# Kernel tuning notes

Hardware: AMD Instinct MI355X
Metric: run time of the kernel (lower is better)

Reference implementation:

```python
import jax, jax.numpy as jnp
import numpy as np
import math

N_HEADS = 12
EPS = 1e-5

def _layernorm(x, w, b):
    # torch .var() is unbiased (ddof=1)
    mean = jnp.mean(x, axis=-1, keepdims=True)
    var = jnp.var(x, axis=-1, keepdims=True, ddof=1)
    return (x - mean) / jnp.sqrt(var + EPS) * w + b

def _gelu_tanh(x):
    c = math.sqrt(2.0 / math.pi)
    return 0.5 * x * (1.0 + jnp.tanh(c * (x + 0.044715 * x * x * x)))

def setup_inputs() -> dict:
    key = jax.random.key(0)
    ks = jax.random.split(key, 6)
    B, T, C = 4, 2048, 768
    s = 0.02
    return {
        "x": jax.random.normal(ks[0], (B, T, C), jnp.float32),
        "ln1_w": jnp.ones((C,), jnp.float32),
        "ln1_b": jnp.zeros((C,), jnp.float32),
        "c_attn_w": jax.random.normal(ks[1], (C, 3 * C), jnp.float32) * s,
        "c_attn_b": jnp.zeros((3 * C,), jnp.float32),
        "c_proj_w": jax.random.normal(ks[2], (C, C), jnp.float32) * s,
        "c_proj_b": jnp.zeros((C,), jnp.float32),
        "ln2_w": jnp.ones((C,), jnp.float32),
        "ln2_b": jnp.zeros((C,), jnp.float32),
        "fc_w": jax.random.normal(ks[3], (C, 4 * C), jnp.float32) * s,
        "fc_b": jnp.zeros((4 * C,), jnp.float32),
        "mproj_w": jax.random.normal(ks[4], (4 * C, C), jnp.float32) * s,
        "mproj_b": jnp.zeros((C,), jnp.float32),
    }

def _attention(x, c_attn_w, c_attn_b, c_proj_w, c_proj_b):
    B, T, C = x.shape
    H = N_HEADS
    D = C // H
    qkv = x @ c_attn_w + c_attn_b  # [B,T,3C]
    q, k, v = jnp.split(qkv, 3, axis=-1)
    q = q.reshape(B, T, H, D).transpose(0, 2, 1, 3)  # [B,H,T,D]
    k = k.reshape(B, T, H, D).transpose(0, 2, 1, 3)
    v = v.reshape(B, T, H, D).transpose(0, 2, 1, 3)
    scores = jnp.einsum("bhqd,bhkd->bhqk", q, k) * (D ** -0.5)  # [B,H,T,T]
    causal = jnp.tril(jnp.ones((T, T), bool))
    scores = jnp.where(causal[None, None], scores, jnp.float32(-jnp.inf))
    attn = jax.nn.softmax(scores, axis=-1)
    out = jnp.einsum("bhqk,bhkd->bhqd", attn, v)  # [B,H,T,D]
    out = out.transpose(0, 2, 1, 3).reshape(B, T, C)
    return out @ c_proj_w + c_proj_b

def reference(x, ln1_w, ln1_b, c_attn_w, c_attn_b, c_proj_w, c_proj_b,
              ln2_w, ln2_b, fc_w, fc_b, mproj_w, mproj_b):
    x = x + _attention(_layernorm(x, ln1_w, ln1_b), c_attn_w, c_attn_b, c_proj_w, c_proj_b)
    h = _gelu_tanh(_layernorm(x, ln2_w, ln2_b) @ fc_w + fc_b)
    return x + h @ mproj_w + mproj_b
```

## Files before the change

kernel.cpp:

```cpp
#include <hip/hip_runtime.h>
#include <hip/hip_bf16.h>
#include <cstdint>

#define BF __hip_bfloat16

typedef __bf16 v8bf __attribute__((ext_vector_type(8)));
typedef float  v4f  __attribute__((ext_vector_type(4)));

__device__ __forceinline__ float tof(BF v) { return __bfloat162float(v); }
__device__ __forceinline__ BF    tob(float v) { return __float2bfloat16(v); }
__device__ __forceinline__ float ldf(float v) { return v; }
__device__ __forceinline__ float ldf(BF v) { return tof(v); }
__device__ __forceinline__ void stv(float* p, float v) { *p = v; }
__device__ __forceinline__ void stv(BF* p, float v) { *p = tob(v); }

__device__ __forceinline__ v4f mfma16(v8bf a, v8bf b, v4f c) {
  return __builtin_amdgcn_mfma_f32_16x16x32_bf16(a, b, c, 0, 0, 0);
}

__device__ __forceinline__ void async16(const BF* g, BF* l) {
  __builtin_amdgcn_global_load_lds((const __attribute__((address_space(1))) void*)g,
                                   (__attribute__((address_space(3))) void*)l, 16, 0, 0);
}

__global__ __launch_bounds__(256) void transpose_k(const float* __restrict__ in,
                                                   BF* __restrict__ out, int R, int C) {
  __shared__ BF t[64][65];
  int tid = threadIdx.x;
  int c0 = blockIdx.x * 64, r0 = blockIdx.y * 64;
#pragma unroll
  for (int i = 0; i < 16; ++i) {
    int idx = i * 256 + tid;
    int rr = idx >> 6, cc = idx & 63;
    t[rr][cc] = tob(in[(size_t)(r0 + rr) * C + c0 + cc]);
  }
  __syncthreads();
#pragma unroll
  for (int i = 0; i < 16; ++i) {
    int idx = i * 256 + tid;
    int rr = idx >> 6, cc = idx & 63;
    out[(size_t)(c0 + rr) * R + r0 + cc] = t[cc][rr];
  }
}

__global__ __launch_bounds__(256) void vtrans_k(const BF* __restrict__ qkv,
                                                BF* __restrict__ vT) {
  __shared__ BF t[64][65];
  int tid = threadIdx.x;
  int t0 = blockIdx.x * 64;
  int bh = blockIdx.y;
  int b = bh / 12, h = bh % 12;
  const BF* src = qkv + (size_t)(b * 2048 + t0) * 2304 + 1536 + h * 64;
#pragma unroll
  for (int i = 0; i < 16; ++i) {
    int idx = i * 256 + tid;
    int rr = idx >> 6, cc = idx & 63;
    t[rr][cc] = src[(size_t)rr * 2304 + cc];
  }
  __syncthreads();
  BF* dst = vT + (size_t)bh * 64 * 2048 + t0;
#pragma unroll
  for (int i = 0; i < 16; ++i) {
    int idx = i * 256 + tid;
    int rr = idx >> 6, cc = idx & 63;
    dst[(size_t)rr * 2048 + cc] = t[cc][rr];
  }
}

template <typename TX>
__global__ __launch_bounds__(256) void ln_k(const TX* __restrict__ x,
                                            const float* __restrict__ w,
                                            const float* __restrict__ bia,
                                            BF* __restrict__ y) {
  int row = blockIdx.x, tid = threadIdx.x;
  const TX* xr = x + (size_t)row * 768;
  float v0 = ldf(xr[tid]), v1 = ldf(xr[tid + 256]), v2 = ldf(xr[tid + 512]);
  float s1 = v0 + v1 + v2;
  float s2 = v0 * v0 + v1 * v1 + v2 * v2;
#pragma unroll
  for (int m = 32; m; m >>= 1) { s1 += __shfl_xor(s1, m); s2 += __shfl_xor(s2, m); }
  __shared__ float rs[4][2];
  int wv = tid >> 6;
  if ((tid & 63) == 0) { rs[wv][0] = s1; rs[wv][1] = s2; }
  __syncthreads();
  s1 = rs[0][0] + rs[1][0] + rs[2][0] + rs[3][0];
  s2 = rs[0][1] + rs[1][1] + rs[2][1] + rs[3][1];
  float mean = s1 * (1.0f / 768.0f);
  float var = fmaxf((s2 - s1 * mean) * (1.0f / 767.0f), 0.0f);
  float rstd = rsqrtf(var + 1e-5f);
  BF* yr = y + (size_t)row * 768;
  yr[tid]       = tob((v0 - mean) * rstd * w[tid]       + bia[tid]);
  yr[tid + 256] = tob((v1 - mean) * rstd * w[tid + 256] + bia[tid + 256]);
  yr[tid + 512] = tob((v2 - mean) * rstd * w[tid + 512] + bia[tid + 512]);
}

__device__ __forceinline__ float gelu_f(float x) {
  float u = 0.7978845608028654f * (x + 0.044715f * x * x * x);
  float e = exp2f(2.8853900817779268f * u);
  return 0.5f * x * (1.0f + (1.0f - 2.0f / (e + 1.0f)));
}

template <int BN, int ACT, bool RESID, typename TR, typename TO>
__global__ __launch_bounds__(256) void gemm_bt_k(
    const BF* __restrict__ A, const BF* __restrict__ Bt, const float* __restrict__ bias,
    const TR* __restrict__ resid, TO* __restrict__ out, int M, int N, int K) {
  constexpr int NW = BN / 32;
  __shared__ __align__(16) BF As[128 * 32];
  __shared__ __align__(16) BF Bs[BN * 32];
  const int tid = threadIdx.x;
  const int w = tid >> 6, lane = tid & 63;
  const int quad = lane >> 4, l16 = lane & 15;
  const int m0 = blockIdx.y * 128, n0 = blockIdx.x * BN;
  const int wm = (w >> 1) * 64, wn = (w & 1) * (BN / 2);
  const int srow = lane >> 2, scol = (lane & 3) * 8;

  v4f acc[4][NW];
#pragma unroll
  for (int i = 0; i < 4; ++i)
#pragma unroll
    for (int j = 0; j < NW; ++j) acc[i][j] = (v4f){0.f, 0.f, 0.f, 0.f};

  for (int k0 = 0; k0 < K; k0 += 32) {
    __syncthreads();
#pragma unroll
    for (int i = 0; i < 2; ++i) {
      int c = w * 2 + i;
      async16(A + (size_t)(m0 + c * 16 + srow) * K + k0 + scol, &As[c * 512]);
    }
    if (BN == 128) {
#pragma unroll
      for (int i = 0; i < 2; ++i) {
        int c = w * 2 + i;
        async16(Bt + (size_t)(n0 + c * 16 + srow) * K + k0 + scol, &Bs[c * 512]);
      }
    } else {
      async16(Bt + (size_t)(n0 + w * 16 + srow) * K + k0 + scol, &Bs[w * 512]);
    }
    __syncthreads();
    v8bf af[4], bfv[NW];
#pragma unroll
    for (int mi = 0; mi < 4; ++mi)
      af[mi] = *(const v8bf*)&As[(wm + mi * 16 + l16) * 32 + quad * 8];
#pragma unroll
    for (int nj = 0; nj < NW; ++nj)
      bfv[nj] = *(const v8bf*)&Bs[(wn + nj * 16 + l16) * 32 + quad * 8];
#pragma unroll
    for (int mi = 0; mi < 4; ++mi)
#pragma unroll
      for (int nj = 0; nj < NW; ++nj)
        acc[mi][nj] = mfma16(af[mi], bfv[nj], acc[mi][nj]);
  }

#pragma unroll
  for (int nj = 0; nj < NW; ++nj) {
    int col = n0 + wn + nj * 16 + l16;
    float bv = bias[col];
#pragma unroll
    for (int mi = 0; mi < 4; ++mi) {
      v4f c = acc[mi][nj];
#pragma unroll
      for (int r = 0; r < 4; ++r) {
        int row = m0 + wm + mi * 16 + quad * 4 + r;
        float v = c[r] + bv;
        if (RESID) v += ldf(resid[(size_t)row * N + col]);
        if (ACT == 1) v = gelu_f(v);
        stv(&out[(size_t)row * N + col], v);
      }
    }
  }
}

__global__ __launch_bounds__(256) void attn_k(const BF* __restrict__ qkv,
                                              const BF* __restrict__ vT,
                                              BF* __restrict__ out) {
  __shared__ __align__(16) BF Ks[64 * 64];
  __shared__ __align__(16) BF Vs[64 * 64];
  __shared__ __align__(16) BF Ps[4][16 * 64];
  const int tid = threadIdx.x;
  const int w = tid >> 6, lane = tid & 63;
  const int quad = lane >> 4, l16 = lane & 15;
  const int bid = blockIdx.x;
  const int qi = 31 - (bid / 48);
  const int bh = bid % 48;
  const int b = bh / 12, h = bh % 12;
  const int q0 = qi * 64;
  const int qf = q0 + w * 16;
  BF* Pw = &Ps[w][0];
  const float L2E = 1.4426950408889634f;

  auto sz = [](int r, int c) { return (r << 6) + (c ^ ((r & 7) << 3)); };

  const BF* qp = qkv + (size_t)(b * 2048 + qf + l16) * 2304 + h * 64;
  v8bf q0v = *(const v8bf*)(qp + quad * 8);
  v8bf q1v = *(const v8bf*)(qp + 32 + quad * 8);
#pragma unroll
  for (int i = 0; i < 8; ++i) {
    q0v[i] = (__bf16)(tof((BF)q0v[i]) * 0.125f);
    q1v[i] = (__bf16)(tof((BF)q1v[i]) * 0.125f);
  }
  v8bf ones;
#pragma unroll
  for (int i = 0; i < 8; ++i) ones[i] = (__bf16)1.0f;

  v4f O[4], S;
#pragma unroll
  for (int j = 0; j < 4; ++j) O[j] = (v4f){0.f, 0.f, 0.f, 0.f};
  S = (v4f){0.f, 0.f, 0.f, 0.f};

  const BF* kg = qkv + (size_t)b * 2048 * 2304 + 768 + h * 64;
  const BF* vg = vT + (size_t)bh * 64 * 2048;
  const int r0 = tid >> 3, c0 = (tid & 7) * 8;
  const int r1 = r0 + 32;
  const int nIter = qi + 1;

  v8bf nk0 = *(const v8bf*)(kg + (size_t)r0 * 2304 + c0);
  v8bf nk1 = *(const v8bf*)(kg + (size_t)r1 * 2304 + c0);
  v8bf nv0 = *(const v8bf*)(vg + (size_t)r0 * 2048 + c0);
  v8bf nv1 = *(const v8bf*)(vg + (size_t)r1 * 2048 + c0);

  for (int t = 0; t < nIter; ++t) {
    const int kt0 = t * 64;
    __syncthreads();
    *(v8bf*)&Ks[sz(r0, c0)] = nk0;
    *(v8bf*)&Ks[sz(r1, c0)] = nk1;
    *(v8bf*)&Vs[sz(r0, c0)] = nv0;
    *(v8bf*)&Vs[sz(r1, c0)] = nv1;
    __syncthreads();
    if (t + 1 < nIter) {
      const int kn = kt0 + 64;
      nk0 = *(const v8bf*)(kg + (size_t)(kn + r0) * 2304 + c0);
      nk1 = *(const v8bf*)(kg + (size_t)(kn + r1) * 2304 + c0);
      nv0 = *(const v8bf*)(vg + (size_t)r0 * 2048 + kn + c0);
      nv1 = *(const v8bf*)(vg + (size_t)r1 * 2048 + kn + c0);
    }
    v4f s[4];
    __builtin_amdgcn_s_setprio(1);
#pragma unroll
    for (int nt = 0; nt < 4; ++nt) {
      v8bf kf0 = *(const v8bf*)&Ks[sz(nt * 16 + l16, quad * 8)];
      v8bf kf1 = *(const v8bf*)&Ks[sz(nt * 16 + l16, 32 + quad * 8)];
      s[nt] = mfma16(q1v, kf1, mfma16(q0v, kf0, (v4f){0.f, 0.f, 0.f, 0.f}));
    }
    __builtin_amdgcn_s_setprio(0);
    if (t < qi) {
#pragma unroll
      for (int nt = 0; nt < 4; ++nt)
#pragma unroll
        for (int r = 0; r < 4; ++r)
          Pw[sz(quad * 4 + r, nt * 16 + l16)] = tob(exp2f(s[nt][r] * L2E));
    } else {
#pragma unroll
      for (int nt = 0; nt < 4; ++nt) {
        int key = kt0 + nt * 16 + l16;
#pragma unroll
        for (int r = 0; r < 4; ++r) {
          int qrow = qf + quad * 4 + r;
          float p = (key <= qrow) ? exp2f(s[nt][r] * L2E) : 0.f;
          Pw[sz(quad * 4 + r, nt * 16 + l16)] = tob(p);
        }
      }
    }
    asm volatile("s_waitcnt lgkmcnt(0)" ::: "memory");
    v8bf p0 = *(const v8bf*)&Pw[sz(l16, quad * 8)];
    v8bf p1 = *(const v8bf*)&Pw[sz(l16, 32 + quad * 8)];
    __builtin_amdgcn_s_setprio(1);
#pragma unroll
    for (int j = 0; j < 4; ++j) {
      v8bf vf0 = *(const v8bf*)&Vs[sz(j * 16 + l16, quad * 8)];
      v8bf vf1 = *(const v8bf*)&Vs[sz(j * 16 + l16, 32 + quad * 8)];
      O[j] = mfma16(p1, vf1, mfma16(p0, vf0, O[j]));
    }
    S = mfma16(p1, ones, mfma16(p0, ones, S));
    __builtin_amdgcn_s_setprio(0);
  }

#pragma unroll
  for (int r = 0; r < 4; ++r) {
    float inv = 1.0f / S[r];
    int row = b * 2048 + qf + quad * 4 + r;
    BF* op = out + (size_t)row * 768 + h * 64 + l16;
#pragma unroll
    for (int j = 0; j < 4; ++j) op[j * 16] = tob(O[j][r] * inv);
  }
}

extern "C" void kernel_launch(void* const* d_in, const int* in_sizes, int n_in,
                              void* d_out, int out_size, void* d_ws, size_t ws_size,
                              hipStream_t stream) {
  const float* x        = (const float*)d_in[0];
  const float* ln1_w    = (const float*)d_in[1];
  const float* ln1_b    = (const float*)d_in[2];
  const float* c_attn_w = (const float*)d_in[3];
  const float* c_attn_b = (const float*)d_in[4];
  const float* c_proj_w = (const float*)d_in[5];
  const float* c_proj_b = (const float*)d_in[6];
  const float* ln2_w    = (const float*)d_in[7];
  const float* ln2_b    = (const float*)d_in[8];
  const float* fc_w     = (const float*)d_in[9];
  const float* fc_b     = (const float*)d_in[10];
  const float* mproj_w  = (const float*)d_in[11];
  const float* mproj_b  = (const float*)d_in[12];
  float* out = (float*)d_out;
  char* wsb = (char*)d_ws;
  dim3 blk(256);

  BF* vT = (BF*)((char*)d_out + 12582912);

  const size_t NEED_BIG = 89653248;
  if (ws_size >= NEED_BIG) {
    BF* qkv      = (BF*)(wsb);
    BF* hbuf     = (BF*)(wsb);
    BF* x2       = (BF*)(wsb + 50331648);
    BF* wT_attn  = (BF*)(wsb + 62914560);
    BF* wT_proj  = (BF*)(wsb + 66453504);
    BF* wT_fc    = (BF*)(wsb + 67633152);
    BF* wT_mproj = (BF*)(wsb + 72351744);
    BF* lnbuf    = (BF*)(wsb + 77070336);
    BF* attnout  = (BF*)d_out;

    transpose_k<<<dim3(36, 12), blk, 0, stream>>>(c_attn_w, wT_attn, 768, 2304);
    transpose_k<<<dim3(12, 12), blk, 0, stream>>>(c_proj_w, wT_proj, 768, 768);
    transpose_k<<<dim3(48, 12), blk, 0, stream>>>(fc_w, wT_fc, 768, 3072);
    transpose_k<<<dim3(12, 48), blk, 0, stream>>>(mproj_w, wT_mproj, 3072, 768);

    ln_k<float><<<8192, blk, 0, stream>>>(x, ln1_w, ln1_b, lnbuf);
    gemm_bt_k<128, 0, false, float, BF><<<dim3(18, 64), blk, 0, stream>>>(
        lnbuf, wT_attn, c_attn_b, (const float*)nullptr, qkv, 8192, 2304, 768);
    vtrans_k<<<dim3(32, 48), blk, 0, stream>>>(qkv, vT);
    attn_k<<<dim3(1536), blk, 0, stream>>>(qkv, vT, attnout);
    gemm_bt_k<64, 0, true, float, BF><<<dim3(12, 64), blk, 0, stream>>>(
        attnout, wT_proj, c_proj_b, x, x2, 8192, 768, 768);
    ln_k<BF><<<8192, blk, 0, stream>>>(x2, ln2_w, ln2_b, lnbuf);
    gemm_bt_k<128, 1, false, float, BF><<<dim3(24, 64), blk, 0, stream>>>(
        lnbuf, wT_fc, fc_b, (const float*)nullptr, hbuf, 8192, 3072, 768);
    gemm_bt_k<64, 0, true, BF, float><<<dim3(12, 64), blk, 0, stream>>>(
        hbuf, wT_mproj, mproj_b, x2, out, 8192, 768, 3072);
  } else {
    BF* ws       = (BF*)d_ws;
    BF* qkv      = ws;
    BF* attnout  = ws + (size_t)18874368;
    BF* wT_attn  = attnout;
    BF* x2       = ws;
    BF* wT_proj  = ws + (size_t)6291456;
    BF* wT_fc    = ws + (size_t)6881280;
    BF* wT_mproj = ws + (size_t)9240576;
    BF* hbuf     = ws + (size_t)11599872;
    BF* lnbuf    = (BF*)d_out;

    transpose_k<<<dim3(36, 12), blk, 0, stream>>>(c_attn_w, wT_attn, 768, 2304);
    ln_k<float><<<8192, blk, 0, stream>>>(x, ln1_w, ln1_b, lnbuf);
    gemm_bt_k<128, 0, false, float, BF><<<dim3(18, 64), blk, 0, stream>>>(
        lnbuf, wT_attn, c_attn_b, (const float*)nullptr, qkv, 8192, 2304, 768);
    vtrans_k<<<dim3(32, 48), blk, 0, stream>>>(qkv, vT);
    attn_k<<<dim3(1536), blk, 0, stream>>>(qkv, vT, attnout);
    transpose_k<<<dim3(12, 12), blk, 0, stream>>>(c_proj_w, wT_proj, 768, 768);
    gemm_bt_k<64, 0, true, float, BF><<<dim3(12, 64), blk, 0, stream>>>(
        attnout, wT_proj, c_proj_b, x, x2, 8192, 768, 768);
    ln_k<BF><<<8192, blk, 0, stream>>>(x2, ln2_w, ln2_b, lnbuf);
    transpose_k<<<dim3(48, 12), blk, 0, stream>>>(fc_w, wT_fc, 768, 3072);
    transpose_k<<<dim3(12, 48), blk, 0, stream>>>(mproj_w, wT_mproj, 3072, 768);
    for (int half = 1; half >= 0; --half) {
      size_t r0 = (size_t)half * 4096;
      gemm_bt_k<128, 1, false, float, BF><<<dim3(24, 32), blk, 0, stream>>>(
          lnbuf + r0 * 768, wT_fc, fc_b, (const float*)nullptr, hbuf, 4096, 3072, 768);
      gemm_bt_k<64, 0, true, BF, float><<<dim3(12, 32), blk, 0, stream>>>(
          hbuf, wT_mproj, mproj_b, x2 + r0 * 768, out + r0 * 768, 4096, 768, 3072);
    }
  }
}
```

Baseline: 413.4 us.

## Double-buffer GEMM LDS tiles with K=64, XOR swizzle, and grid remapping

```diff
diff --git a/kernel.cpp b/kernel.cpp
--- a/kernel.cpp
+++ b/kernel.cpp
@@ -105,14 +105,19 @@
     const BF* __restrict__ A, const BF* __restrict__ Bt, const float* __restrict__ bias,
     const TR* __restrict__ resid, TO* __restrict__ out, int M, int N, int K) {
   constexpr int NW = BN / 32;
-  __shared__ __align__(16) BF As[128 * 32];
-  __shared__ __align__(16) BF Bs[BN * 32];
+  __shared__ __align__(16) BF As[2][128 * 64];
+  __shared__ __align__(16) BF Bs[2][BN * 64];
   const int tid = threadIdx.x;
   const int w = tid >> 6, lane = tid & 63;
   const int quad = lane >> 4, l16 = lane & 15;
-  const int m0 = blockIdx.y * 128, n0 = blockIdx.x * BN;
+  const int gx = gridDim.x;
+  const int nwg = gx * gridDim.y;
+  const int lid = blockIdx.y * gx + blockIdx.x;
+  const int swz = (lid & 7) * (nwg >> 3) + (lid >> 3);
+  const int m0 = (swz / gx) * 128, n0 = (swz % gx) * BN;
   const int wm = (w >> 1) * 64, wn = (w & 1) * (BN / 2);
-  const int srow = lane >> 2, scol = (lane & 3) * 8;
+  const int sr = lane >> 3;
+  const int sc = ((lane & 7) ^ sr) * 8;
 
   v4f acc[4][NW];
 #pragma unroll
@@ -120,35 +125,55 @@
 #pragma unroll
     for (int j = 0; j < NW; ++j) acc[i][j] = (v4f){0.f, 0.f, 0.f, 0.f};
 
-  for (int k0 = 0; k0 < K; k0 += 32) {
+  auto stage = [&](int bsel, int k0) {
+#pragma unroll
+    for (int i = 0; i < 4; ++i) {
+      int r0 = w * 32 + i * 8;
+      async16(A + (size_t)(m0 + r0 + sr) * K + k0 + sc, &As[bsel][r0 * 64]);
+    }
+    if (BN == 128) {
+#pragma unroll
+      for (int i = 0; i < 4; ++i) {
+        int r0 = w * 32 + i * 8;
+        async16(Bt + (size_t)(n0 + r0 + sr) * K + k0 + sc, &Bs[bsel][r0 * 64]);
+      }
+    } else {
+#pragma unroll
+      for (int i = 0; i < 2; ++i) {
+        int r0 = w * 16 + i * 8;
+        async16(Bt + (size_t)(n0 + r0 + sr) * K + k0 + sc, &Bs[bsel][r0 * 64]);
+      }
+    }
+  };
+
+  const int nkt = K >> 6;
+  stage(0, 0);
+  __syncthreads();
+  for (int kt = 0; kt < nkt; ++kt) {
+    const int cur = kt & 1;
+    if (kt + 1 < nkt) stage(cur ^ 1, (kt + 1) << 6);
+#pragma unroll
+    for (int kk = 0; kk < 2; ++kk) {
+      v8bf af[4], bfv[NW];
+#pragma unroll
+      for (int mi = 0; mi < 4; ++mi) {
+        int row = wm + mi * 16 + l16;
+        af[mi] = *(const v8bf*)&As[cur][row * 64 + (((kk * 4 + quad) ^ (row & 7)) * 8)];
+      }
+#pragma unroll
+      for (int nj = 0; nj < NW; ++nj) {
+        int row = wn + nj * 16 + l16;
+        bfv[nj] = *(const v8bf*)&Bs[cur][row * 64 + (((kk * 4 + quad) ^ (row & 7)) * 8)];
+      }
+      __builtin_amdgcn_s_setprio(1);
+#pragma unroll
+      for (int mi = 0; mi < 4; ++mi)
+#pragma unroll
+        for (int nj = 0; nj < NW; ++nj)
+          acc[mi][nj] = mfma16(af[mi], bfv[nj], acc[mi][nj]);
+      __builtin_amdgcn_s_setprio(0);
+    }
     __syncthreads();
-#pragma unroll
-    for (int i = 0; i < 2; ++i) {
-      int c = w * 2 + i;
-      async16(A + (size_t)(m0 + c * 16 + srow) * K + k0 + scol, &As[c * 512]);
-    }
-    if (BN == 128) {
-#pragma unroll
-      for (int i = 0; i < 2; ++i) {
-        int c = w * 2 + i;
-        async16(Bt + (size_t)(n0 + c * 16 + srow) * K + k0 + scol, &Bs[c * 512]);
-      }
-    } else {
-      async16(Bt + (size_t)(n0 + w * 16 + srow) * K + k0 + scol, &Bs[w * 512]);
-    }
-    __syncthreads();
-    v8bf af[4], bfv[NW];
-#pragma unroll
-    for (int mi = 0; mi < 4; ++mi)
-      af[mi] = *(const v8bf*)&As[(wm + mi * 16 + l16) * 32 + quad * 8];
-#pragma unroll
-    for (int nj = 0; nj < NW; ++nj)
-      bfv[nj] = *(const v8bf*)&Bs[(wn + nj * 16 + l16) * 32 + quad * 8];
-#pragma unroll
-    for (int mi = 0; mi < 4; ++mi)
-#pragma unroll
-      for (int nj = 0; nj < NW; ++nj)
-        acc[mi][nj] = mfma16(af[mi], bfv[nj], acc[mi][nj]);
   }
 
 #pragma unroll
```

New measurement: 368.5 us. 1.12x faster.
